# Performance work log

Measured on AMD Instinct MI355X. Metric: run time of the kernel, lower is better.

The kernel has to match this reference:

```python
import jax, jax.numpy as jnp
import numpy as np
from jax.lax import associative_scan

B, S, D, F, G = 4, 4096, 1024, 4096, 32
EPS = 1e-6


def setup_inputs() -> dict:
    key = jax.random.key(0)
    ks = jax.random.split(key, 16)
    xn = lambda k, shp: jax.random.normal(k, shp, jnp.float32) / np.sqrt(shp[0])
    return {
        "x": jax.random.normal(ks[0], (B, S, D), jnp.float32),
        "Wq": xn(ks[1], (D, D)),
        "Wk": xn(ks[2], (D, D)),
        "Wv": xn(ks[3], (D, D)),
        "Wa": xn(ks[4], (D, 2 * D)),
        "Wg": xn(ks[5], (D, D)),
        "Wo": xn(ks[6], (D, D)),
        "gn_scale": jnp.ones((D,), jnp.float32),
        "gn_bias": jnp.zeros((D,), jnp.float32),
        "ln1_scale": jnp.ones((D,), jnp.float32),
        "ln1_bias": jnp.zeros((D,), jnp.float32),
        "W1": xn(ks[7], (D, F)),
        "b1": jax.random.normal(ks[8], (F,), jnp.float32) * 1e-6,
        "W2": xn(ks[9], (F, D)),
        "b2": jax.random.normal(ks[10], (D,), jnp.float32) * 1e-6,
        "ln2_scale": jnp.ones((D,), jnp.float32),
        "ln2_bias": jnp.zeros((D,), jnp.float32),
    }


def _gate_loop(k, v, q, a):
    # max-headed GateLoop: per-channel complex linear recurrence
    # h_t = a_t * h_{t-1} + k_t * v_t ; y_t = q_t * h_t
    kv = (k * v).astype(jnp.complex64)
    def op(e1, e2):
        a1, x1 = e1
        a2, x2 = e2
        return (a1 * a2, a2 * x1 + x2)
    _, h = associative_scan(op, (a, kv), axis=1)
    return q.astype(jnp.complex64) * h


def _layernorm(x, scale, bias):
    mu = jnp.mean(x, axis=-1, keepdims=True)
    var = jnp.mean(jnp.square(x - mu), axis=-1, keepdims=True)
    return (x - mu) * jax.lax.rsqrt(var + EPS) * scale + bias


def _groupnorm_complex(y, scale, bias):
    # flax GroupNorm on complex input: mean is complex, var = E|y|^2 - |E y|^2 (real)
    b, s, d = y.shape
    yr = y.reshape(b, s, G, d // G)
    mean = jnp.mean(yr, axis=(1, 3), keepdims=True)
    mean2 = jnp.mean(yr.real ** 2 + yr.imag ** 2, axis=(1, 3), keepdims=True)
    var = mean2 - (mean.real ** 2 + mean.imag ** 2)
    yn = (yr - mean) * jax.lax.rsqrt(var + EPS)
    return yn.reshape(b, s, d) * scale + bias


def reference(x, Wq, Wk, Wv, Wa, Wg, Wo, gn_scale, gn_bias, ln1_scale, ln1_bias,
              W1, b1, W2, b2, ln2_scale, ln2_bias):
    q = x @ Wq
    k = x @ Wk
    v = x @ Wv
    a = x @ Wa
    a_real, a_imag = jnp.split(a, 2, axis=-1)
    a_c = a_real + 1j * a_imag
    mag = jnp.abs(a_c)
    phase = jnp.angle(a_c)
    a_c = jax.nn.sigmoid(mag) * jnp.exp(1j * phase)

    g = (x @ Wg).astype(jnp.complex64)

    y = _gate_loop(k, v, q, a_c)                       # [B,S,D] complex64
    y = _groupnorm_complex(y, gn_scale, gn_bias)
    silu_g = g / (1.0 + jnp.exp(-g))                    # complex silu
    y = y * silu_g
    y = (y @ Wo.astype(jnp.complex64)).real

    x = _layernorm(x + y, ln1_scale, ln1_bias)
    h = jax.nn.gelu(x @ W1 + b1)
    out = x + (h @ W2 + b2)
    return _layernorm(out, ln2_scale, ln2_bias)
```

## Files before the change

kernel.cpp:

```cpp
#include <hip/hip_runtime.h>
#include <cstdint>
#include <cstddef>


#define EPSN 1e-6f

typedef _Float16 f16;
typedef _Float16 f16x8 __attribute__((ext_vector_type(8)));
typedef _Float16 f16x4 __attribute__((ext_vector_type(4)));
typedef float    f32x4 __attribute__((ext_vector_type(4)));

static constexpr int    Bb     = 4;
static constexpr int    Ss     = 4096;
static constexpr int    Dd     = 1024;
static constexpr int    Ff     = 4096;
static constexpr int    Mrows  = Bb * Ss;
static constexpr size_t MD     = (size_t)Mrows * Dd;
static constexpr int    CHUNKS = 64;
static constexpr int    CLEN   = Ss / CHUNKS;
static constexpr int    BD     = Bb * Dd;
static constexpr int    CBD    = CHUNKS * BD;
static constexpr size_t MiB    = 1024 * 1024;
static constexpr int    PLD    = 4096;

__device__ __forceinline__ float fast_sigmoid(float x) {
    float e = __builtin_amdgcn_exp2f(-1.4426950408889634f * x);
    return __builtin_amdgcn_rcpf(1.0f + e);
}
__device__ __forceinline__ float gelu_tanh(float x) {
    float z = 0.7978845608028654f * (x + 0.044715f * x * x * x);
    z = fminf(fmaxf(z, -10.0f), 10.0f);
    float e = __builtin_amdgcn_exp2f(2.885390081777927f * z);
    float t = (e - 1.0f) * __builtin_amdgcn_rcpf(e + 1.0f);
    return 0.5f * x * (1.0f + t);
}

__device__ __forceinline__ void async16(const void* g, void* l) {
    __builtin_amdgcn_global_load_lds(
        (const __attribute__((address_space(1))) unsigned int*)(uintptr_t)g,
        (__attribute__((address_space(3))) unsigned int*)(uintptr_t)l,
        16, 0, 0);
}

template <int EPI, typename TC>
__global__ __launch_bounds__(512, 2) void mgemm_k(const f16* __restrict__ A, int lda,
                                                  const f16* __restrict__ Bt,
                                                  TC* __restrict__ C, int ldc,
                                                  int M, int N, int K,
                                                  const float* __restrict__ bias) {
    __shared__ f16 sA[2 * 256 * 64];
    __shared__ f16 sB[2 * 256 * 64];
    const int tid  = threadIdx.x;
    const int wave = tid >> 6;
    const int lane = tid & 63;

    const int gx  = gridDim.x;
    const int nwg = gx * gridDim.y;
    int bid = blockIdx.y * gx + blockIdx.x;
    bid = (bid & 7) * (nwg >> 3) + (bid >> 3);
    const int bm = (bid / gx) * 256;
    const int bn = (bid % gx) * 256;

    const int rw = (wave >> 2) * 128;
    const int cw = (wave & 3) * 64;

    const int swz  = (((lane & 7) ^ (lane >> 3)) & 7) * 8;
    const int srow = wave * 16 + (lane >> 3);
    const f16* gA0 = A  + (size_t)(bm + srow) * lda + swz;
    const f16* gB0 = Bt + (size_t)(bn + srow) * K   + swz;

    f32x4 acc[8][4] = {};

    const int fr   = lane & 15;
    const int off0 = (((lane >> 4) ^ lane) & 7) * 8;

    const int NT = K >> 6;

#define STG(dst, gp, ld, kOff, h, g)                                           \
    async16((gp) + (size_t)((h) * 128 + (g) * 8) * (ld) + (kOff),              \
            (dst) + ((h) * 128 + wave * 16 + (g) * 8) * 64)

#define LDA4(ib, buf)                                                          \
    _Pragma("unroll") for (int i = 0; i < 4; ++i) {                            \
        const int row_ = (rw + ((ib) + i) * 16 + fr) * 64;                     \
        a_[i][0] = *(const f16x8*)&(buf)[row_ + off0];                         \
        a_[i][1] = *(const f16x8*)&(buf)[row_ + (off0 ^ 32)];                  \
    }
#define LDB2(arr, jb, buf)                                                     \
    _Pragma("unroll") for (int j = 0; j < 2; ++j) {                            \
        const int row_ = (cw + ((jb) + j) * 16 + fr) * 64;                     \
        arr[j][0] = *(const f16x8*)&(buf)[row_ + off0];                        \
        arr[j][1] = *(const f16x8*)&(buf)[row_ + (off0 ^ 32)];                 \
    }
#define MMQ(iq, jq, barr)                                                      \
    __builtin_amdgcn_s_setprio(1);                                             \
    _Pragma("unroll") for (int i = 0; i < 4; ++i)                              \
        _Pragma("unroll") for (int j = 0; j < 2; ++j)                          \
            _Pragma("unroll") for (int kk = 0; kk < 2; ++kk)                   \
                acc[(iq) + i][(jq) + j] = __builtin_amdgcn_mfma_f32_16x16x32_f16( \
                    a_[i][kk], barr[j][kk], acc[(iq) + i][(jq) + j], 0, 0, 0); \
    __builtin_amdgcn_s_setprio(0);

    STG(sA, gA0, lda, 0, 0, 0); STG(sA, gA0, lda, 0, 0, 1);
    STG(sA, gA0, lda, 0, 1, 0); STG(sA, gA0, lda, 0, 1, 1);
    STG(sB, gB0, K,   0, 0, 0); STG(sB, gB0, K,   0, 0, 1);
    STG(sB, gB0, K,   0, 1, 0); STG(sB, gB0, K,   0, 1, 1);
    asm volatile("s_waitcnt vmcnt(0)" ::: "memory");
    __builtin_amdgcn_s_barrier();

    for (int t = 0; t < NT; ++t) {
        const f16* rdA = sA + (t & 1) * 16384;
        const f16* rdB = sB + (t & 1) * 16384;
        f16* stA = sA + ((t + 1) & 1) * 16384;
        f16* stB = sB + ((t + 1) & 1) * 16384;
        const int kS = (t + 1) * 64;
        const bool doSt = (t + 1) < NT;
        f16x8 a_[4][2], bA[2][2], bB[2][2];

        LDA4(0, rdA)
        LDB2(bA, 0, rdB)
        if (doSt) {
            STG(stA, gA0, lda, kS, 0, 0); STG(stA, gA0, lda, kS, 0, 1);
            STG(stA, gA0, lda, kS, 1, 0); STG(stA, gA0, lda, kS, 1, 1);
        }
        __builtin_amdgcn_s_barrier();
        MMQ(0, 0, bA)
        __builtin_amdgcn_s_barrier();

        LDB2(bB, 2, rdB)
        if (doSt) {
            STG(stB, gB0, K, kS, 0, 0); STG(stB, gB0, K, kS, 0, 1);
            STG(stB, gB0, K, kS, 1, 0); STG(stB, gB0, K, kS, 1, 1);
        }
        __builtin_amdgcn_s_barrier();
        MMQ(0, 2, bB)
        __builtin_amdgcn_s_barrier();

        LDA4(4, rdA)
        __builtin_amdgcn_s_barrier();
        MMQ(4, 2, bB)
        __builtin_amdgcn_s_barrier();

        asm volatile("s_waitcnt vmcnt(0)" ::: "memory");
        __builtin_amdgcn_s_barrier();
        MMQ(4, 0, bA)
        __builtin_amdgcn_s_barrier();
    }
#undef STG
#undef LDA4
#undef LDB2
#undef MMQ

    const int er = (lane >> 4) * 4;
    const int ec = lane & 15;
#pragma unroll
    for (int i = 0; i < 8; ++i) {
#pragma unroll
        for (int j = 0; j < 4; ++j) {
            const int col = bn + cw + j * 16 + ec;
#pragma unroll
            for (int r = 0; r < 4; ++r) {
                const size_t row = (size_t)(bm + rw + i * 16 + er + r);
                float o = acc[i][j][r];
                if (EPI == 1 || EPI == 2) o += bias[col];
                if (EPI == 1) o = gelu_tanh(o);
                if (sizeof(TC) == 4) ((float*)C)[row * ldc + col] = o;
                else                 ((f16*)C)[row * ldc + col] = (f16)o;
            }
        }
    }
}

__global__ __launch_bounds__(256) void wtrans_k(const float* __restrict__ W,
                                                f16* __restrict__ Wt,
                                                int K, int N) {
    __shared__ float t[32][33];
    const int n0 = blockIdx.x * 32, k0 = blockIdx.y * 32;
    const int tx = threadIdx.x & 31, ty = threadIdx.x >> 5;
#pragma unroll
    for (int i = 0; i < 32; i += 8)
        t[ty + i][tx] = W[(size_t)(k0 + ty + i) * N + n0 + tx];
    __syncthreads();
#pragma unroll
    for (int i = 0; i < 32; i += 8)
        Wt[(size_t)(n0 + ty + i) * K + k0 + tx] = (f16)t[tx][ty + i];
}

__global__ __launch_bounds__(256) void f2h_k(const float* __restrict__ x,
                                             f16* __restrict__ xh) {
    size_t i = ((size_t)blockIdx.x * 256 + threadIdx.x) * 4;
    float4 v = *(const float4*)&x[i];
    f16x4 s;
    s.x = (f16)v.x; s.y = (f16)v.y; s.z = (f16)v.z; s.w = (f16)v.w;
    *(f16x4*)&xh[i] = s;
}

__global__ __launch_bounds__(256) void a_transform_k(f16* __restrict__ a2d) {
    size_t gid = (size_t)blockIdx.x * 256 + threadIdx.x;
    int    j8  = (int)(gid & 127) * 8;
    size_t row = gid >> 7;
    f16x8 vr = *(f16x8*)&a2d[row * 2048 + j8];
    f16x8 vi = *(f16x8*)&a2d[row * 2048 + 1024 + j8];
#pragma unroll
    for (int i = 0; i < 8; ++i) {
        float ar = (float)vr[i], ai = (float)vi[i];
        float mag = sqrtf(ar * ar + ai * ai);
        float sg  = fast_sigmoid(mag);
        float re, im;
        if (mag > 1e-30f) { float s = sg * __builtin_amdgcn_rcpf(mag); re = ar * s; im = ai * s; }
        else              { re = sg; im = 0.0f; }
        vr[i] = (f16)re; vi[i] = (f16)im;
    }
    *(f16x8*)&a2d[row * 2048 + j8]        = vr;
    *(f16x8*)&a2d[row * 2048 + 1024 + j8] = vi;
}

__global__ __launch_bounds__(256) void scan_pass1_k(const f16* __restrict__ a2d,
                                                    const f16* __restrict__ P,
                                                    float4* __restrict__ chunk) {
    int tid = blockIdx.x * 256 + threadIdx.x;
    int d   = tid & 1023;
    int t1  = tid >> 10;
    int b   = t1 & 3;
    int c   = t1 >> 2;
    int t0  = c * CLEN;
    int rbase = b * Ss;
    float Are = 1.0f, Aim = 0.0f, Hre = 0.0f, Him = 0.0f;
    for (int t = t0; t < t0 + CLEN; ++t) {
        int r = rbase + t;
        float are = (float)a2d[(size_t)r * 2048 + d];
        float aim = (float)a2d[(size_t)r * 2048 + 1024 + d];
        float kvv = (float)P[(size_t)r * PLD + 1024 + d]
                  * (float)P[(size_t)r * PLD + 2048 + d];
        float hre = are * Hre - aim * Him + kvv;
        float him = are * Him + aim * Hre;
        Hre = hre; Him = him;
        float pre = are * Are - aim * Aim;
        float pim = are * Aim + aim * Are;
        Are = pre; Aim = pim;
    }
    chunk[tid] = make_float4(Are, Aim, Hre, Him);
}

__global__ __launch_bounds__(256) void scan_pass2_k(const float4* __restrict__ chunk,
                                                    float2* __restrict__ carry,
                                                    float* __restrict__ stats) {
    int tid = blockIdx.x * blockDim.x + threadIdx.x;
    if (tid < 512) stats[tid] = 0.0f;
    float hre = 0.0f, him = 0.0f;
    for (int c = 0; c < CHUNKS; ++c) {
        int task = c * BD + tid;
        float4 ch = chunk[task];
        carry[task] = make_float2(hre, him);
        float nre = ch.x * hre - ch.y * him + ch.z;
        float nim = ch.x * him + ch.y * hre + ch.w;
        hre = nre; him = nim;
    }
}

__global__ __launch_bounds__(256) void scan_pass3_k(const f16* __restrict__ a2d,
                                                    f16* __restrict__ P,
                                                    const float2* __restrict__ carry,
                                                    float* __restrict__ stats) {
    int tid = blockIdx.x * 256 + threadIdx.x;
    int d   = tid & 1023;
    int t1  = tid >> 10;
    int b   = t1 & 3;
    int c   = t1 >> 2;
    int t0  = c * CLEN;
    int rbase = b * Ss;
    float2 cr = carry[tid];
    float hre = cr.x, him = cr.y;
    float sre = 0.0f, sim = 0.0f, s2 = 0.0f;
    for (int t = t0; t < t0 + CLEN; ++t) {
        int r = rbase + t;
        float are = (float)a2d[(size_t)r * 2048 + d];
        float aim = (float)a2d[(size_t)r * 2048 + 1024 + d];
        float kvv = (float)P[(size_t)r * PLD + 1024 + d]
                  * (float)P[(size_t)r * PLD + 2048 + d];
        float nre = are * hre - aim * him + kvv;
        float nim = are * him + aim * hre;
        hre = nre; him = nim;
        float qv  = (float)P[(size_t)r * PLD + d];
        float yr_ = qv * hre;
        float yi_ = qv * him;
        P[(size_t)r * PLD + d] = (f16)yr_;
        sre += yr_; sim += yi_; s2 += yr_ * yr_ + yi_ * yi_;
    }
#pragma unroll
    for (int off = 16; off > 0; off >>= 1) {
        sre += __shfl_down(sre, off, 32);
        sim += __shfl_down(sim, off, 32);
        s2  += __shfl_down(s2,  off, 32);
    }
    if ((threadIdx.x & 31) == 0) {
        int idx = (b * 32 + (d >> 5)) * 4;
        atomicAdd(&stats[idx + 0], sre);
        atomicAdd(&stats[idx + 1], sim);
        atomicAdd(&stats[idx + 2], s2);
    }
}

__global__ __launch_bounds__(256) void gn_gate_k(f16* __restrict__ P,
                                                 const float* __restrict__ stats,
                                                 const float* __restrict__ gn_scale,
                                                 const float* __restrict__ gn_bias) {
    size_t gid = (size_t)blockIdx.x * 256 + threadIdx.x;
    int d8  = (int)(gid & 127) * 8;
    int row = (int)(gid >> 7);
    int b   = row >> 12;
    int grp = d8 >> 5;
    const float* st = &stats[(b * 32 + grp) * 4];
    const float invN = 1.0f / 131072.0f;
    float mre = st[0] * invN;
    float mim = st[1] * invN;
    float var = st[2] * invN - mre * mre - mim * mim;
    float rstd = rsqrtf(var + EPSN);
    f16x8 yv = *(f16x8*)&P[(size_t)row * PLD + d8];
    f16x8 gv = *(const f16x8*)&P[(size_t)row * PLD + 3072 + d8];
#pragma unroll
    for (int i = 0; i < 8; ++i) {
        float re = ((float)yv[i] - mre) * rstd * gn_scale[d8 + i] + gn_bias[d8 + i];
        float gx = (float)gv[i];
        yv[i] = (f16)(re * gx * fast_sigmoid(gx));
    }
    *(f16x8*)&P[(size_t)row * PLD + d8] = yv;
}

__device__ __forceinline__ float ldf(const float* p, size_t i) { return p[i]; }
__device__ __forceinline__ float ldf(const f16* p, size_t i)   { return (float)p[i]; }
__device__ __forceinline__ void  stf(float* p, size_t i, float v) { p[i] = v; }
__device__ __forceinline__ void  stf(f16* p, size_t i, float v)   { p[i] = (f16)v; }

__device__ __forceinline__ float block_reduce_sum(float v, float* s4, int tid) {
#pragma unroll
    for (int off = 32; off > 0; off >>= 1) v += __shfl_down(v, off, 64);
    __syncthreads();
    if ((tid & 63) == 0) s4[tid >> 6] = v;
    __syncthreads();
    return s4[0] + s4[1] + s4[2] + s4[3];
}

template <typename TA, typename TB, typename TO>
__global__ __launch_bounds__(256) void ln_k(const TA* __restrict__ a,
                                            const TB* __restrict__ b,
                                            const float* __restrict__ scale,
                                            const float* __restrict__ bias,
                                            TO* __restrict__ out) {
    __shared__ float s4[4];
    int row = blockIdx.x;
    size_t base = (size_t)row * 1024;
    int tid = threadIdx.x;
    float v[4];
    float s = 0.0f;
#pragma unroll
    for (int i = 0; i < 4; ++i) {
        int d = tid + i * 256;
        v[i] = ldf(a, base + d) + ldf(b, base + d);
        s += v[i];
    }
    float mu = block_reduce_sum(s, s4, tid) * (1.0f / 1024.0f);
    float s2 = 0.0f;
#pragma unroll
    for (int i = 0; i < 4; ++i) {
        float dv = v[i] - mu;
        s2 += dv * dv;
    }
    float var = block_reduce_sum(s2, s4, tid) * (1.0f / 1024.0f);
    float rstd = rsqrtf(var + EPSN);
#pragma unroll
    for (int i = 0; i < 4; ++i) {
        int d = tid + i * 256;
        stf(out, base + d, (v[i] - mu) * rstd * scale[d] + bias[d]);
    }
}

extern "C" void kernel_launch(void* const* d_in, const int* in_sizes, int n_in,
                              void* d_out, int out_size, void* d_ws, size_t ws_size,
                              hipStream_t stream) {
    const float* x        = (const float*)d_in[0];
    const float* Wq       = (const float*)d_in[1];
    const float* Wk       = (const float*)d_in[2];
    const float* Wv       = (const float*)d_in[3];
    const float* Wa       = (const float*)d_in[4];
    const float* Wg       = (const float*)d_in[5];
    const float* Wo       = (const float*)d_in[6];
    const float* gn_scale = (const float*)d_in[7];
    const float* gn_bias  = (const float*)d_in[8];
    const float* ln1_s    = (const float*)d_in[9];
    const float* ln1_b    = (const float*)d_in[10];
    const float* W1       = (const float*)d_in[11];
    const float* b1       = (const float*)d_in[12];
    const float* W2       = (const float*)d_in[13];
    const float* b2       = (const float*)d_in[14];
    const float* ln2_s    = (const float*)d_in[15];
    const float* ln2_b    = (const float*)d_in[16];
    float* out = (float*)d_out;

    char* base = (char*)d_ws;
    f16* W1T = (f16*)(base + 0 * MiB);
    f16* W2T = (f16*)(base + 8 * MiB);
    f16* PWT = (f16*)(base + 16 * MiB);
    f16* WoT = (f16*)(base + 24 * MiB);
    f16* WaT = (f16*)(base + 26 * MiB);
    float4* chunk = (float4*)(base + 30 * MiB);
    float2* carry = (float2*)(base + 34 * MiB);
    float*  stats = (float*)(base + 36 * MiB);
    f16* xb  = (f16*)(base + 37 * MiB);
    f16* P   = (f16*)(base + 69 * MiB);
    f16*   ab = (f16*)d_out;
    f16*   yo = (f16*)d_out;
    f16*   x1 = xb;
    f16*   h1 = P;
    float* h2 = (float*)d_out;

    dim3 blk(256);
    dim3 gblk(512);

    f2h_k<<<Mrows, blk, 0, stream>>>(x, xb);
    wtrans_k<<<dim3(128, 32), blk, 0, stream>>>(W1, W1T, Dd, Ff);
    wtrans_k<<<dim3(32, 128), blk, 0, stream>>>(W2, W2T, Ff, Dd);
    wtrans_k<<<dim3(32, 32),  blk, 0, stream>>>(Wq, PWT + 0u * 1048576, Dd, Dd);
    wtrans_k<<<dim3(32, 32),  blk, 0, stream>>>(Wk, PWT + 1u * 1048576, Dd, Dd);
    wtrans_k<<<dim3(32, 32),  blk, 0, stream>>>(Wv, PWT + 2u * 1048576, Dd, Dd);
    wtrans_k<<<dim3(32, 32),  blk, 0, stream>>>(Wg, PWT + 3u * 1048576, Dd, Dd);
    wtrans_k<<<dim3(32, 32),  blk, 0, stream>>>(Wo, WoT, Dd, Dd);
    wtrans_k<<<dim3(64, 32),  blk, 0, stream>>>(Wa, WaT, Dd, 2 * Dd);

    mgemm_k<0, f16><<<dim3(16, 64), gblk, 0, stream>>>(xb, Dd, PWT, P, PLD, Mrows, 4096, Dd, nullptr);
    mgemm_k<0, f16><<<dim3(8, 64),  gblk, 0, stream>>>(xb, Dd, WaT, ab, 2048, Mrows, 2048, Dd, nullptr);

    a_transform_k<<<MD / (256 * 8), blk, 0, stream>>>(ab);

    scan_pass1_k<<<CBD / 256, blk, 0, stream>>>(ab, P, chunk);
    scan_pass2_k<<<BD / 256, blk, 0, stream>>>(chunk, carry, stats);
    scan_pass3_k<<<CBD / 256, blk, 0, stream>>>(ab, P, carry, stats);

    gn_gate_k<<<MD / (256 * 8), blk, 0, stream>>>(P, stats, gn_scale, gn_bias);

    mgemm_k<0, f16><<<dim3(4, 64), gblk, 0, stream>>>(P, PLD, WoT, yo, Dd, Mrows, Dd, Dd, nullptr);
    ln_k<float, f16, f16><<<Mrows, blk, 0, stream>>>(x, yo, ln1_s, ln1_b, x1);

    mgemm_k<1, f16  ><<<dim3(16, 64), gblk, 0, stream>>>(x1, Dd, W1T, h1, Ff, Mrows, Ff, Dd, b1);
    mgemm_k<2, float><<<dim3(4, 64),  gblk, 0, stream>>>(h1, Ff, W2T, h2, Dd, Mrows, Dd, Ff, b2);

    ln_k<f16, float, float><<<Mrows, blk, 0, stream>>>(x1, h2, ln2_s, ln2_b, out);
}
```

Measured before the change: 893.8 us.

## Split GEMM K-tile into two 32-wide halves with finer-grained async staging

The shared-memory tiles are re-laid out as two K-halves of 32 columns, each with its own 4-way XOR swizzle. The main loop now loads all four B fragments plus four A fragments per half and issues 16 MFMAs per quarter. The next tile's global-to-LDS loads are interleaved per half and gated by partial vmcnt waits instead of one full drain. The aim is to overlap the async copies with compute and cut fragment register pressure. In exchange, the vmcnt counts and the new swizzle must exactly match the issued loads, or the kernel will race or hit bank conflicts.

```diff
diff --git a/kernel.cpp b/kernel.cpp
--- a/kernel.cpp
+++ b/kernel.cpp
@@ -48,8 +48,8 @@
                                                   TC* __restrict__ C, int ldc,
                                                   int M, int N, int K,
                                                   const float* __restrict__ bias) {
-    __shared__ f16 sA[2 * 256 * 64];
-    __shared__ f16 sB[2 * 256 * 64];
+    __shared__ f16 sA[2 * 16384];
+    __shared__ f16 sB[2 * 16384];
     const int tid  = threadIdx.x;
     const int wave = tid >> 6;
     const int lane = tid & 63;
@@ -64,91 +64,89 @@
     const int rw = (wave >> 2) * 128;
     const int cw = (wave & 3) * 64;
 
-    const int swz  = (((lane & 7) ^ (lane >> 3)) & 7) * 8;
-    const int srow = wave * 16 + (lane >> 3);
-    const f16* gA0 = A  + (size_t)(bm + srow) * lda + swz;
-    const f16* gB0 = Bt + (size_t)(bn + srow) * K   + swz;
+    const int swzcF = (((lane & 3) ^ (lane >> 3)) & 3) * 8;
+    const f16* gA0 = A  + (size_t)(bm + wave * 16 + (lane >> 2)) * lda + swzcF;
+    const f16* gB0 = Bt + (size_t)(bn + wave * 16 + (lane >> 2)) * K   + swzcF;
 
     f32x4 acc[8][4] = {};
 
     const int fr   = lane & 15;
-    const int off0 = (((lane >> 4) ^ lane) & 7) * 8;
+    const int off0 = (((lane >> 4) ^ (lane >> 1)) & 3) * 8;
 
     const int NT = K >> 6;
 
-#define STG(dst, gp, ld, kOff, h, g)                                           \
-    async16((gp) + (size_t)((h) * 128 + (g) * 8) * (ld) + (kOff),              \
-            (dst) + ((h) * 128 + wave * 16 + (g) * 8) * 64)
-
-#define LDA4(ib, buf)                                                          \
-    _Pragma("unroll") for (int i = 0; i < 4; ++i) {                            \
-        const int row_ = (rw + ((ib) + i) * 16 + fr) * 64;                     \
-        a_[i][0] = *(const f16x8*)&(buf)[row_ + off0];                         \
-        a_[i][1] = *(const f16x8*)&(buf)[row_ + (off0 ^ 32)];                  \
-    }
-#define LDB2(arr, jb, buf)                                                     \
-    _Pragma("unroll") for (int j = 0; j < 2; ++j) {                            \
-        const int row_ = (cw + ((jb) + j) * 16 + fr) * 64;                     \
-        arr[j][0] = *(const f16x8*)&(buf)[row_ + off0];                        \
-        arr[j][1] = *(const f16x8*)&(buf)[row_ + (off0 ^ 32)];                 \
-    }
-#define MMQ(iq, jq, barr)                                                      \
+#define STGA(SB, KOFF, KK, G)                                                  \
+    async16(gA0 + (size_t)(G) * 128 * lda + (KOFF) + (KK) * 32,                \
+            sA + (SB) * 16384 + (KK) * 8192 + ((G) * 128 + wave * 16) * 32)
+#define STGB(SB, KOFF, KK, G)                                                  \
+    async16(gB0 + (size_t)(G) * 128 * K + (KOFF) + (KK) * 32,                  \
+            sB + (SB) * 16384 + (KK) * 8192 + ((G) * 128 + wave * 16) * 32)
+
+#define LDA4(IH, KK, BUF)                                                      \
+    _Pragma("unroll") for (int i = 0; i < 4; ++i)                              \
+        a_[i] = *(const f16x8*)&sA[(BUF) * 16384 + (KK) * 8192 +               \
+                                   (rw + ((IH) + i) * 16 + fr) * 32 + off0];
+#define LDB4(KK, BUF)                                                          \
+    _Pragma("unroll") for (int j = 0; j < 4; ++j)                              \
+        b_[j] = *(const f16x8*)&sB[(BUF) * 16384 + (KK) * 8192 +               \
+                                   (cw + j * 16 + fr) * 32 + off0];
+#define MMQ(IH)                                                                \
     __builtin_amdgcn_s_setprio(1);                                             \
     _Pragma("unroll") for (int i = 0; i < 4; ++i)                              \
-        _Pragma("unroll") for (int j = 0; j < 2; ++j)                          \
-            _Pragma("unroll") for (int kk = 0; kk < 2; ++kk)                   \
-                acc[(iq) + i][(jq) + j] = __builtin_amdgcn_mfma_f32_16x16x32_f16( \
-                    a_[i][kk], barr[j][kk], acc[(iq) + i][(jq) + j], 0, 0, 0); \
+        _Pragma("unroll") for (int j = 0; j < 4; ++j)                          \
+            acc[(IH) + i][j] = __builtin_amdgcn_mfma_f32_16x16x32_f16(         \
+                a_[i], b_[j], acc[(IH) + i][j], 0, 0, 0);                      \
     __builtin_amdgcn_s_setprio(0);
 
-    STG(sA, gA0, lda, 0, 0, 0); STG(sA, gA0, lda, 0, 0, 1);
-    STG(sA, gA0, lda, 0, 1, 0); STG(sA, gA0, lda, 0, 1, 1);
-    STG(sB, gB0, K,   0, 0, 0); STG(sB, gB0, K,   0, 0, 1);
-    STG(sB, gB0, K,   0, 1, 0); STG(sB, gB0, K,   0, 1, 1);
+    STGA(0, 0, 0, 0); STGA(0, 0, 0, 1); STGA(0, 0, 1, 0); STGA(0, 0, 1, 1);
+    STGB(0, 0, 0, 0); STGB(0, 0, 0, 1); STGB(0, 0, 1, 0); STGB(0, 0, 1, 1);
     asm volatile("s_waitcnt vmcnt(0)" ::: "memory");
     __builtin_amdgcn_s_barrier();
 
     for (int t = 0; t < NT; ++t) {
-        const f16* rdA = sA + (t & 1) * 16384;
-        const f16* rdB = sB + (t & 1) * 16384;
-        f16* stA = sA + ((t + 1) & 1) * 16384;
-        f16* stB = sB + ((t + 1) & 1) * 16384;
+        const int rd = t & 1, st = rd ^ 1;
         const int kS = (t + 1) * 64;
         const bool doSt = (t + 1) < NT;
-        f16x8 a_[4][2], bA[2][2], bB[2][2];
-
-        LDA4(0, rdA)
-        LDB2(bA, 0, rdB)
+        f16x8 a_[4], b_[4];
+
+        LDB4(0, rd)
+        LDA4(0, 0, rd)
+        if (doSt) { STGA(st, kS, 0, 0); STGA(st, kS, 0, 1); }
+        __builtin_amdgcn_s_barrier();
+        MMQ(0)
+        __builtin_amdgcn_s_barrier();
+
+        LDA4(4, 0, rd)
         if (doSt) {
-            STG(stA, gA0, lda, kS, 0, 0); STG(stA, gA0, lda, kS, 0, 1);
-            STG(stA, gA0, lda, kS, 1, 0); STG(stA, gA0, lda, kS, 1, 1);
+            STGB(st, kS, 0, 0); STGB(st, kS, 0, 1);
+            asm volatile("s_waitcnt vmcnt(4)" ::: "memory");
+        } else {
+            asm volatile("s_waitcnt vmcnt(0)" ::: "memory");
         }
         __builtin_amdgcn_s_barrier();
-        MMQ(0, 0, bA)
-        __builtin_amdgcn_s_barrier();
-
-        LDB2(bB, 2, rdB)
+        MMQ(4)
+        __builtin_amdgcn_s_barrier();
+
+        LDB4(1, rd)
+        LDA4(0, 1, rd)
+        if (doSt) { STGA(st, kS, 1, 0); STGA(st, kS, 1, 1); }
+        __builtin_amdgcn_s_barrier();
+        MMQ(0)
+        __builtin_amdgcn_s_barrier();
+
+        LDA4(4, 1, rd)
         if (doSt) {
-            STG(stB, gB0, K, kS, 0, 0); STG(stB, gB0, K, kS, 0, 1);
-            STG(stB, gB0, K, kS, 1, 0); STG(stB, gB0, K, kS, 1, 1);
+            STGB(st, kS, 1, 0); STGB(st, kS, 1, 1);
+            asm volatile("s_waitcnt vmcnt(4)" ::: "memory");
         }
         __builtin_amdgcn_s_barrier();
-        MMQ(0, 2, bB)
-        __builtin_amdgcn_s_barrier();
-
-        LDA4(4, rdA)
-        __builtin_amdgcn_s_barrier();
-        MMQ(4, 2, bB)
-        __builtin_amdgcn_s_barrier();
-
-        asm volatile("s_waitcnt vmcnt(0)" ::: "memory");
-        __builtin_amdgcn_s_barrier();
-        MMQ(4, 0, bA)
-        __builtin_amdgcn_s_barrier();
-    }
-#undef STG
+        MMQ(4)
+        __builtin_amdgcn_s_barrier();
+    }
+#undef STGA
+#undef STGB
 #undef LDA4
-#undef LDB2
+#undef LDB4
 #undef MMQ
 
     const int er = (lane >> 4) * 4;
```

Result: no change. 892.1 us (-0.2%).
